# Optimization experiments

Hardware: AMD Instinct MI355X
Metric: run time of the kernel (lower is better)

Reference implementation:

```python
import jax, jax.numpy as jnp
import numpy as np

N = 50000      # nodes
E = 600000     # edges (avg degree 12)
D_IN = 16      # node_input_size
D = 128        # hidden_size
H = 4          # num_heads
DH = D // H
L = 4          # message_passing_num
D_FF = 512     # 4*hidden FFN expansion
D_OUT = 3      # output_size


def setup_inputs() -> dict:
    key = jax.random.key(0)
    ks = iter(jax.random.split(key, 32))
    def w(shape, fan_in):
        return jax.random.normal(next(ks), shape, jnp.float32) / np.float32(np.sqrt(fan_in))
    return {
        "features": jax.random.normal(next(ks), (N, D_IN), jnp.float32),
        "senders": jax.random.randint(next(ks), (E,), 0, N),
        "receivers": jax.random.randint(next(ks), (E,), 0, N),
        "enc_w1": w((D_IN, D), D_IN), "enc_b1": jnp.zeros((D,), jnp.float32),
        "enc_w2": w((D, D), D),       "enc_b2": jnp.zeros((D,), jnp.float32),
        "wq": w((L, D, D), D), "wk": w((L, D, D), D),
        "wv": w((L, D, D), D), "wo": w((L, D, D), D),
        "ln1_s": jnp.ones((L, D), jnp.float32), "ln1_b": jnp.zeros((L, D), jnp.float32),
        "ffn_w1": w((L, D, D_FF), D), "ffn_b1": jnp.zeros((L, D_FF), jnp.float32),
        "ffn_w2": w((L, D_FF, D), D_FF), "ffn_b2": jnp.zeros((L, D), jnp.float32),
        "ln2_s": jnp.ones((L, D), jnp.float32), "ln2_b": jnp.zeros((L, D), jnp.float32),
        "dec_w1": w((D, D_OUT), D), "dec_b1": jnp.zeros((D_OUT,), jnp.float32),
        "dec_w2": w((D_OUT, D_OUT), D_OUT), "dec_b2": jnp.zeros((D_OUT,), jnp.float32),
    }


def _ln(x, s, b):
    mu = x.mean(-1, keepdims=True)
    var = ((x - mu) ** 2).mean(-1, keepdims=True)
    return (x - mu) * jax.lax.rsqrt(var + 1e-5) * s + b


def _graph_mha(x, senders, receivers, wq, wk, wv, wo):
    # Adjacency-masked attention done sparsely over the edge list
    # (equivalent to softmax over the BCOO adjacency pattern).
    n = x.shape[0]
    q = (x @ wq).reshape(n, H, DH)
    k = (x @ wk).reshape(n, H, DH)
    v = (x @ wv).reshape(n, H, DH)
    scores = (q[receivers] * k[senders]).sum(-1) / np.float32(np.sqrt(DH))  # [E,H]
    m = jax.ops.segment_max(scores, receivers, num_segments=n)             # [N,H]
    m = jnp.where(jnp.isfinite(m), m, 0.0)
    a = jnp.exp(scores - m[receivers])                                      # [E,H]
    denom = jax.ops.segment_sum(a, receivers, num_segments=n)              # [N,H]
    msg = jax.ops.segment_sum(a[:, :, None] * v[senders], receivers, num_segments=n)  # [N,H,DH]
    out = (msg / (denom[:, :, None] + 1e-9)).reshape(n, D)
    return out @ wo


def reference(features, senders, receivers,
              enc_w1, enc_b1, enc_w2, enc_b2,
              wq, wk, wv, wo, ln1_s, ln1_b,
              ffn_w1, ffn_b1, ffn_w2, ffn_b2, ln2_s, ln2_b,
              dec_w1, dec_b1, dec_w2, dec_b2):
    # encode
    x = jnp.maximum(features @ enc_w1 + enc_b1, 0.0) @ enc_w2 + enc_b2     # [N,D]
    # process: L pre-LN sparse-attention transformer blocks
    for l in range(L):
        h = _ln(x, ln1_s[l], ln1_b[l])
        x = x + _graph_mha(h, senders, receivers, wq[l], wk[l], wv[l], wo[l])
        h = _ln(x, ln2_s[l], ln2_b[l])
        x = x + jnp.maximum(h @ ffn_w1[l] + ffn_b1[l], 0.0) @ ffn_w2[l] + ffn_b2[l]
    # decode
    return jnp.maximum(x @ dec_w1 + dec_b1, 0.0) @ dec_w2 + dec_b2         # [N,D_OUT]
```

## Files before the change

kernel.cpp:

```cpp
#include <hip/hip_runtime.h>
#include <hip/hip_bf16.h>
#include <math.h>

#define D     128
#define NHEAD 4
#define DH    32
#define DFF   512
#define DIN   16
#define MAXDEG 64
#define TN    16

typedef __attribute__((ext_vector_type(8))) short bf16x8;
typedef __attribute__((ext_vector_type(4))) float f32x4;
typedef __hip_bfloat16 bf16;

#define QSCALE_L2E 0.2550348838f


#define WAITV(N) asm volatile("s_waitcnt vmcnt(" #N ")" ::: "memory")
#define WAITLGKM asm volatile("s_waitcnt lgkmcnt(0)" ::: "memory")
#define FENCE()  asm volatile("" ::: "memory")
#define BAR() do { FENCE(); __builtin_amdgcn_s_barrier(); FENCE(); } while (0)

__device__ __forceinline__ void gll16(const bf16* g, bf16* l) {
    __builtin_amdgcn_global_load_lds((__attribute__((address_space(1))) void*)g,
                                     (__attribute__((address_space(3))) void*)l,
                                     16, 0, 0);
}

__device__ __forceinline__ ushort bfbits(float f) {
    __hip_bfloat16 b = __float2bfloat16(f);
    return *(ushort*)&b;
}

__global__ void k_fill(const int* __restrict__ recv, const int* __restrict__ senders,
                       int* __restrict__ deg, int* __restrict__ eid, int E) {
    int e = blockIdx.x * blockDim.x + threadIdx.x;
    if (e >= E) return;
    int r = recv[e];
    int pos = atomicAdd(&deg[r], 1);
    if (pos < MAXDEG) eid[r * MAXDEG + pos] = senders[e];
}

__global__ void k_wt(const float* __restrict__ wq, const float* __restrict__ wk,
                     const float* __restrict__ wv, const float* __restrict__ wo,
                     const float* __restrict__ w1, const float* __restrict__ w2,
                     const float* __restrict__ encw2,
                     bf16* __restrict__ wqkvT, bf16* __restrict__ woT,
                     bf16* __restrict__ w1T, bf16* __restrict__ w2T,
                     bf16* __restrict__ encw2T, int* __restrict__ deg,
                     int* __restrict__ eid, int N) {
    int r = blockIdx.y;
    if (r == 25) {
        int tot = N + N * MAXDEG;
        for (int i = blockIdx.x * blockDim.x + threadIdx.x; i < tot;
             i += 256 * 256) {
            if (i < N) deg[i] = 0;
            else eid[i - N] = 0;
        }
        return;
    }
    const float* src; bf16* dst; int K, Nout;
    if (r < 12) {
        int l = r / 3, sel = r % 3;
        src = (sel == 0 ? wq : sel == 1 ? wk : wv) + (size_t)l * D * D;
        dst = wqkvT + (size_t)l * 3 * D * D + (size_t)sel * D * D;
        K = D; Nout = D;
    } else if (r < 16) {
        int l = r - 12;
        src = wo + (size_t)l * D * D; dst = woT + (size_t)l * D * D; K = D; Nout = D;
    } else if (r < 20) {
        int l = r - 16;
        src = w1 + (size_t)l * D * DFF; dst = w1T + (size_t)l * D * DFF; K = D; Nout = DFF;
    } else if (r < 24) {
        int l = r - 20;
        src = w2 + (size_t)l * DFF * D; dst = w2T + (size_t)l * DFF * D; K = DFF; Nout = D;
    } else {
        src = encw2; dst = encw2T; K = D; Nout = D;
    }
    int total = K * Nout;
    int i = blockIdx.x * blockDim.x + threadIdx.x;
    if (i >= total) return;
    int k = i / Nout, j = i % Nout;
    dst[(size_t)j * K + k] = __float2bfloat16(src[i]);
}

__device__ __forceinline__ void load_afrag(const bf16* A, int arow, int quad,
                                           int N, bf16x8* afr) {
    const bf16* ab = A + (size_t)arow * D + quad * 8;
#pragma unroll
    for (int i = 0; i < 4; i++) {
        uint4 v = make_uint4(0u, 0u, 0u, 0u);
        if (arow < N) v = *(const uint4*)(ab + i * 32);
        afr[i] = *(bf16x8*)&v;
    }
}

__device__ __forceinline__ void stage_q(bf16* lb, const bf16* src, int rs,
                                        int wave, int lane) {
#pragma unroll
    for (int k = 0; k < 2; k++) {
        int gidx = (wave * 2 + k) * 64 + lane;
        int r = gidx >> 2, gL = gidx & 3;
        gll16(src + (size_t)r * rs + ((gL ^ ((r >> 1) & 3)) * 8),
              lb + (size_t)(wave * 2 + k) * 512);
    }
}

template<int OP>
__global__ __launch_bounds__(256) void k_gemm(
        const bf16* __restrict__ A, const bf16* __restrict__ Bt,
        const float* __restrict__ bias,
        const float* __restrict__ lns, const float* __restrict__ lnb,
        float* x, bf16* outB, int N) {
    __shared__ alignas(16) bf16 Wq4[4][32 * 128];
    int m0 = blockIdx.x * 64;
    int t = threadIdx.x;
    int wave = t >> 6, lane = t & 63;
    int quad = lane >> 4, l16 = lane & 15;
    int wm = wave * 16;
    int rowb = m0 + wm + quad * 4;

    float xv[8][4];
    if (OP == 2) {
#pragma unroll
        for (int j = 0; j < 8; j++)
#pragma unroll
            for (int r = 0; r < 4; r++) {
                int gr = rowb + r;
                xv[j][r] = (gr < N) ? x[(size_t)gr * D + j * 16 + l16] : 0.f;
            }
    }
    bf16x8 afr[4];
    load_afrag(A, m0 + wm + l16, quad, N, afr);
    FENCE();
#pragma unroll
    for (int p = 0; p < 4; p++) {
        stage_q(&Wq4[p][0], Bt + p * 32, 128, wave, lane);
        FENCE();
    }

    int wswz = (quad ^ ((l16 >> 1) & 3)) * 8;
    f32x4 acc[8];
#pragma unroll
    for (int j = 0; j < 8; j++) acc[j] = (f32x4){0.f, 0.f, 0.f, 0.f};
#pragma unroll
    for (int s = 0; s < 4; s++) {
        if (s == 0) { WAITV(6); } else if (s == 1) { WAITV(4); }
        else if (s == 2) { WAITV(2); } else { WAITV(0); }
        BAR();
        const bf16* Wb = &Wq4[s][0];
        __builtin_amdgcn_s_setprio(1);
#pragma unroll
        for (int j = 0; j < 8; j++) {
            const bf16* wp = Wb + (size_t)(j * 16 + l16) * 32 + wswz;
            acc[j] = __builtin_amdgcn_mfma_f32_16x16x32_bf16(
                afr[s], *(const bf16x8*)wp, acc[j], 0, 0, 0);
        }
        __builtin_amdgcn_s_setprio(0);
    }

    float bv[8];
    if (OP == 5) {
#pragma unroll
        for (int j = 0; j < 8; j++) bv[j] = bias[j * 16 + l16];
    }
#pragma unroll
    for (int j = 0; j < 8; j++) {
#pragma unroll
        for (int r = 0; r < 4; r++) {
            int gr = rowb + r;
            if (gr >= N) continue;
            float val = acc[j][r];
            if (OP == 5) val += bv[j];
            if (OP == 2) val += xv[j][r];
            acc[j][r] = val;
        }
    }
    float lsv[8], lbv[8];
#pragma unroll
    for (int j = 0; j < 8; j++) {
        lsv[j] = lns[j * 16 + l16];
        lbv[j] = lnb[j * 16 + l16];
    }
#pragma unroll
    for (int r = 0; r < 4; r++) {
        float s1 = 0.f, s2 = 0.f;
#pragma unroll
        for (int j = 0; j < 8; j++) {
            float v = acc[j][r];
            s1 += v; s2 += v * v;
        }
        s1 += __shfl_xor(s1, 1, 64);  s2 += __shfl_xor(s2, 1, 64);
        s1 += __shfl_xor(s1, 2, 64);  s2 += __shfl_xor(s2, 2, 64);
        s1 += __shfl_xor(s1, 4, 64);  s2 += __shfl_xor(s2, 4, 64);
        s1 += __shfl_xor(s1, 8, 64);  s2 += __shfl_xor(s2, 8, 64);
        float mu = s1 * (1.f / 128.f);
        float var = s2 * (1.f / 128.f) - mu * mu;
        float rinv = rsqrtf(fmaxf(var, 0.f) + 1e-5f);
        int gr = rowb + r;
        if (gr >= N) continue;
#pragma unroll
        for (int j = 0; j < 8; j++) {
            int col = j * 16 + l16;
            float v = acc[j][r];
            x[(size_t)gr * D + col] = v;
            outB[(size_t)gr * D + col] =
                __float2bfloat16((v - mu) * rinv * lsv[j] + lbv[j]);
        }
    }
}

__device__ __forceinline__ void stage_qkv_q(int ts, const bf16* wqkvT,
                                            bf16* Wb6, int wave, int lane) {
    int tsel = ts >> 2, p = ts & 3;
    size_t off = (tsel == 0) ? (size_t)D * D
               : (tsel == 1) ? (size_t)2 * D * D : 0;
    stage_q(Wb6 + (size_t)(ts % 6) * (32 * 128), wqkvT + off + p * 32, 128,
            wave, lane);
}

__global__ __launch_bounds__(256) void k_qkv(
        const bf16* __restrict__ hb, const bf16* __restrict__ wqkvT,
        bf16* __restrict__ qb, bf16* __restrict__ kvb, int N) {
    __shared__ alignas(16) bf16 Wb6[6][32 * 128];
    int m0 = blockIdx.x * 64;
    int t = threadIdx.x;
    int wave = t >> 6, lane = t & 63;
    int quad = lane >> 4, l16 = lane & 15;
    int wm = wave * 16;
    int rowb = m0 + wm + quad * 4;

    bf16x8 afr[4];
    load_afrag(hb, m0 + wm + l16, quad, N, afr);
    FENCE();
    stage_qkv_q(0, wqkvT, &Wb6[0][0], wave, lane); FENCE();
    stage_qkv_q(1, wqkvT, &Wb6[0][0], wave, lane); FENCE();
    stage_qkv_q(2, wqkvT, &Wb6[0][0], wave, lane); FENCE();
    stage_qkv_q(3, wqkvT, &Wb6[0][0], wave, lane); FENCE();

    int wswz = (quad ^ ((l16 >> 1) & 3)) * 8;
    f32x4 accK[8], accV[8], accQ[8];

#pragma unroll
    for (int s = 0; s < 12; s++) {
        if (s + 4 < 12) {
            stage_qkv_q(s + 4, wqkvT, &Wb6[0][0], wave, lane);
            FENCE();
        }
        if (s < 8)        { WAITV(8); }
        else if (s == 8)  { WAITV(6); }
        else if (s == 9)  { WAITV(4); }
        else if (s == 10) { WAITV(2); }
        else              { WAITV(0); }
        BAR();
        const bf16* Wb = &Wb6[0][0] + (size_t)(s % 6) * (32 * 128);
        int q = s & 3;
        __builtin_amdgcn_s_setprio(1);
#pragma unroll
        for (int j = 0; j < 8; j++) {
            const bf16* wp = Wb + (size_t)(j * 16 + l16) * 32 + wswz;
            if (s < 4) {
                if (q == 0) accK[j] = (f32x4){0.f, 0.f, 0.f, 0.f};
                accK[j] = __builtin_amdgcn_mfma_f32_16x16x32_bf16(
                    afr[q], *(const bf16x8*)wp, accK[j], 0, 0, 0);
            } else if (s < 8) {
                if (q == 0) accV[j] = (f32x4){0.f, 0.f, 0.f, 0.f};
                accV[j] = __builtin_amdgcn_mfma_f32_16x16x32_bf16(
                    afr[q], *(const bf16x8*)wp, accV[j], 0, 0, 0);
            } else {
                if (q == 0) accQ[j] = (f32x4){0.f, 0.f, 0.f, 0.f};
                accQ[j] = __builtin_amdgcn_mfma_f32_16x16x32_bf16(
                    afr[q], *(const bf16x8*)wp, accQ[j], 0, 0, 0);
            }
        }
        __builtin_amdgcn_s_setprio(0);
    }

#pragma unroll
    for (int j = 0; j < 8; j++) {
        int col = j * 16 + l16;
#pragma unroll
        for (int r = 0; r < 4; r++) {
            int gr = rowb + r;
            if (gr >= N) continue;
            uint kv = (uint)bfbits(accK[j][r]) | ((uint)bfbits(accV[j][r]) << 16);
            *(uint*)&kvb[((size_t)gr * D + col) * 2] = kv;
            qb[(size_t)gr * D + col] = __float2bfloat16(accQ[j][r] * QSCALE_L2E);
        }
    }
}

__device__ __forceinline__ void stage_ffn_q(int ts, const bf16* w1T,
                                            const bf16* w2T, bf16* Wb6,
                                            int wave, int lane) {
    int c = ts >> 3, p = ts & 7;
    const bf16* src; int rs;
    if (p < 4) { src = w1T + (size_t)(c * 128) * 128 + p * 32;       rs = 128; }
    else       { src = w2T + (size_t)(c * 128) + (p - 4) * 32;       rs = DFF; }
    stage_q(Wb6 + (size_t)(ts % 6) * (32 * 128), src, rs, wave, lane);
}

template<int MODE>
__global__ __launch_bounds__(256) void k_ffn(
        const bf16* __restrict__ hb, const bf16* __restrict__ w1T,
        const float* __restrict__ b1,
        const bf16* __restrict__ w2T, const float* __restrict__ b2,
        const float* __restrict__ lns, const float* __restrict__ lnb,
        const float* __restrict__ dw1, const float* __restrict__ db1,
        const float* __restrict__ dw2, const float* __restrict__ db2,
        float* x, bf16* outB, float* out, int N) {
    __shared__ alignas(16) bf16 Wb6[6][32 * 128];
    __shared__ alignas(16) bf16 Hsm[64 * 128];
    int m0 = blockIdx.x * 64;
    int t = threadIdx.x;
    int wave = t >> 6, lane = t & 63;
    int quad = lane >> 4, l16 = lane & 15;
    int wm = wave * 16;
    int rowb = m0 + wm + quad * 4;

    float b1pre[4][8];
#pragma unroll
    for (int c2 = 0; c2 < 4; c2++)
#pragma unroll
        for (int j = 0; j < 8; j++) b1pre[c2][j] = b1[c2 * 128 + j * 16 + l16];

    bf16x8 afr[4];
    load_afrag(hb, m0 + wm + l16, quad, N, afr);
    FENCE();
    stage_ffn_q(0, w1T, w2T, &Wb6[0][0], wave, lane); FENCE();
    stage_ffn_q(1, w1T, w2T, &Wb6[0][0], wave, lane); FENCE();
    stage_ffn_q(2, w1T, w2T, &Wb6[0][0], wave, lane); FENCE();
    stage_ffn_q(3, w1T, w2T, &Wb6[0][0], wave, lane); FENCE();

    f32x4 acc2[8], accP[8];
#pragma unroll
    for (int j = 0; j < 8; j++) acc2[j] = (f32x4){0.f, 0.f, 0.f, 0.f};
    float xv[8][4];

    int wswz = (quad ^ ((l16 >> 1) & 3)) * 8;

#pragma unroll
    for (int s = 0; s < 32; s++) {
        if (s + 4 < 32) {
            stage_ffn_q(s + 4, w1T, w2T, &Wb6[0][0], wave, lane);
            FENCE();
        }
        if (s < 28)       { WAITV(8); }
        else if (s == 28) { WAITV(6); }
        else if (s == 29) { WAITV(4); }
        else if (s == 30) { WAITV(2); }
        else              { WAITV(0); }
        BAR();
        if (s == 31) {
#pragma unroll
            for (int j = 0; j < 8; j++)
#pragma unroll
                for (int r = 0; r < 4; r++) {
                    int gr = min(rowb + r, N - 1);
                    xv[j][r] = x[(size_t)gr * D + j * 16 + l16];
                }
            FENCE();
        }
        const bf16* Wb = &Wb6[0][0] + (size_t)(s % 6) * (32 * 128);
        int c = s >> 3, p = s & 7;
        if (p < 4) {
            if (p == 0) {
#pragma unroll
                for (int j = 0; j < 8; j++) accP[j] = (f32x4){0.f, 0.f, 0.f, 0.f};
            }
            __builtin_amdgcn_s_setprio(1);
#pragma unroll
            for (int j = 0; j < 8; j++) {
                const bf16* wp = Wb + (size_t)(j * 16 + l16) * 32 + wswz;
                accP[j] = __builtin_amdgcn_mfma_f32_16x16x32_bf16(
                    afr[p], *(const bf16x8*)wp, accP[j], 0, 0, 0);
            }
            __builtin_amdgcn_s_setprio(0);
            if (p == 3) {
                int rw = wm + quad * 4;
#pragma unroll
                for (int j = 0; j < 8; j++) {
                    int gb = j * 2 + (l16 >> 3), ce = l16 & 7;
#pragma unroll
                    for (int r = 0; r < 4; r++) {
                        int row = rw + r;
                        Hsm[(size_t)row * 128 + (size_t)((gb ^ (row & 15)) * 8) + ce] =
                            __float2bfloat16(fmaxf(accP[j][r] + b1pre[c][j], 0.f));
                    }
                }
                WAITLGKM;
            }
        } else {
            int kq = p - 4;
            bf16x8 af2 = *(const bf16x8*)(Hsm + (size_t)(wm + l16) * 128
                              + (size_t)(((kq * 4 + quad) ^ l16) * 8));
            __builtin_amdgcn_s_setprio(1);
#pragma unroll
            for (int j = 0; j < 8; j++) {
                const bf16* wp = Wb + (size_t)(j * 16 + l16) * 32 + wswz;
                acc2[j] = __builtin_amdgcn_mfma_f32_16x16x32_bf16(
                    af2, *(const bf16x8*)wp, acc2[j], 0, 0, 0);
            }
            __builtin_amdgcn_s_setprio(0);
        }
    }
    WAITV(0);
    FENCE();

    float bv[8];
#pragma unroll
    for (int j = 0; j < 8; j++) bv[j] = b2[j * 16 + l16];
#pragma unroll
    for (int j = 0; j < 8; j++) {
#pragma unroll
        for (int r = 0; r < 4; r++) {
            int gr = rowb + r;
            if (gr >= N) continue;
            acc2[j][r] += bv[j] + xv[j][r];
        }
    }
    if (MODE == 1) {
        float dw[8][3];
#pragma unroll
        for (int j = 0; j < 8; j++) {
            int col = j * 16 + l16;
#pragma unroll
            for (int cc3 = 0; cc3 < 3; cc3++) dw[j][cc3] = dw1[col * 3 + cc3];
        }
#pragma unroll
        for (int r = 0; r < 4; r++) {
            float s0 = 0.f, s1 = 0.f, s2 = 0.f;
#pragma unroll
            for (int j = 0; j < 8; j++) {
                float v = acc2[j][r];
                s0 += v * dw[j][0]; s1 += v * dw[j][1]; s2 += v * dw[j][2];
            }
            s0 += __shfl_xor(s0, 1, 64); s1 += __shfl_xor(s1, 1, 64); s2 += __shfl_xor(s2, 1, 64);
            s0 += __shfl_xor(s0, 2, 64); s1 += __shfl_xor(s1, 2, 64); s2 += __shfl_xor(s2, 2, 64);
            s0 += __shfl_xor(s0, 4, 64); s1 += __shfl_xor(s1, 4, 64); s2 += __shfl_xor(s2, 4, 64);
            s0 += __shfl_xor(s0, 8, 64); s1 += __shfl_xor(s1, 8, 64); s2 += __shfl_xor(s2, 8, 64);
            int gr = rowb + r;
            if (l16 == 0 && gr < N) {
                float t0 = fmaxf(s0 + db1[0], 0.f);
                float t1 = fmaxf(s1 + db1[1], 0.f);
                float t2 = fmaxf(s2 + db1[2], 0.f);
#pragma unroll
                for (int o = 0; o < 3; o++)
                    out[(size_t)gr * 3 + o] =
                        t0 * dw2[0 * 3 + o] + t1 * dw2[1 * 3 + o] + t2 * dw2[2 * 3 + o] + db2[o];
            }
        }
        return;
    }
    float lsv[8], lbv[8];
#pragma unroll
    for (int j = 0; j < 8; j++) {
        lsv[j] = lns[j * 16 + l16];
        lbv[j] = lnb[j * 16 + l16];
    }
#pragma unroll
    for (int r = 0; r < 4; r++) {
        float s1 = 0.f, s2 = 0.f;
#pragma unroll
        for (int j = 0; j < 8; j++) {
            float v = acc2[j][r];
            s1 += v; s2 += v * v;
        }
        s1 += __shfl_xor(s1, 1, 64);  s2 += __shfl_xor(s2, 1, 64);
        s1 += __shfl_xor(s1, 2, 64);  s2 += __shfl_xor(s2, 2, 64);
        s1 += __shfl_xor(s1, 4, 64);  s2 += __shfl_xor(s2, 4, 64);
        s1 += __shfl_xor(s1, 8, 64);  s2 += __shfl_xor(s2, 8, 64);
        float mu = s1 * (1.f / 128.f);
        float var = s2 * (1.f / 128.f) - mu * mu;
        float rinv = rsqrtf(fmaxf(var, 0.f) + 1e-5f);
        int gr = rowb + r;
        if (gr >= N) continue;
#pragma unroll
        for (int j = 0; j < 8; j++) {
            int col = j * 16 + l16;
            float v = acc2[j][r];
            x[(size_t)gr * D + col] = v;
            outB[(size_t)gr * D + col] = __float2bfloat16((v - mu) * rinv * lsv[j] + lbv[j]);
        }
    }
}

__global__ void k_enc1(const float* __restrict__ feat,
                       const float* __restrict__ w1, const float* __restrict__ b1,
                       bf16* __restrict__ hb, int N) {
    __shared__ float fsh[TN][DIN];
    int n0 = blockIdx.x * TN;
    int j = threadIdx.x;
    int nvalid = min(TN, N - n0);
    for (int idx = j; idx < TN * DIN; idx += 128) {
        int n = idx / DIN, i = idx % DIN;
        fsh[n][i] = (n < nvalid) ? feat[(n0 + n) * DIN + i] : 0.f;
    }
    __syncthreads();
    float bb = b1[j];
#pragma unroll
    for (int n = 0; n < TN; n++) {
        float a = bb;
#pragma unroll
        for (int i = 0; i < DIN; i++) a += fsh[n][i] * w1[i * D + j];
        if (n < nvalid) hb[(size_t)(n0 + n) * D + j] = __float2bfloat16(fmaxf(a, 0.f));
    }
}

__device__ __forceinline__ void attn_edge(uint4 w, bool v, float4 qv,
                                          float& l, float& a0, float& a1,
                                          float& a2, float& a3) {
    float k0 = __uint_as_float(w.x << 16), v0 = __uint_as_float(w.x & 0xFFFF0000u);
    float k1 = __uint_as_float(w.y << 16), v1 = __uint_as_float(w.y & 0xFFFF0000u);
    float k2 = __uint_as_float(w.z << 16), v2 = __uint_as_float(w.z & 0xFFFF0000u);
    float k3 = __uint_as_float(w.w << 16), v3 = __uint_as_float(w.w & 0xFFFF0000u);
    float p = qv.x * k0 + qv.y * k1 + qv.z * k2 + qv.w * k3;
    p += __shfl_xor(p, 1, 64);
    p += __shfl_xor(p, 2, 64);
    p += __shfl_xor(p, 4, 64);
    float e = v ? exp2f(p) : 0.f;
    l += e;
    a0 += e * v0; a1 += e * v1; a2 += e * v2; a3 += e * v3;
}

__device__ __forceinline__ float4 unpackq(uint2 qw) {
    float4 qv;
    qv.x = __uint_as_float(qw.x << 16);
    qv.y = __uint_as_float(qw.x & 0xFFFF0000u);
    qv.z = __uint_as_float(qw.y << 16);
    qv.w = __uint_as_float(qw.y & 0xFFFF0000u);
    return qv;
}

__global__ __launch_bounds__(256) void k_attn(
        const bf16* __restrict__ qb, const uint* __restrict__ kvb,
        const int* __restrict__ deg, const int* __restrict__ eid,
        bf16* __restrict__ out, int N) {
    int wave = threadIdx.x >> 6, lane = threadIdx.x & 63;
    int g = lane & 7, h = (lane >> 3) & 3, slot = lane >> 5;
    int d0 = h * 32 + g * 4;
    int rbase = blockIdx.x * 16 + wave * 4;
    if (rbase >= N) return;
    const uint* kvbase = kvb + d0;

    int ssN[8];
    {
        const int* row = eid + (size_t)rbase * MAXDEG;
#pragma unroll
        for (int u = 0; u < 8; u++) ssN[u] = row[u * 2 + slot];
    }
    int cntN = min(deg[rbase], MAXDEG);
    float4 qvN = unpackq(*(const uint2*)(qb + (size_t)rbase * D + d0));

#pragma unroll
    for (int i = 0; i < 4; i++) {
        int r = rbase + i;
        if (r >= N) return;
        int cnt = cntN; float4 qv = qvN;
        uint4 w[8];
#pragma unroll
        for (int u = 0; u < 8; u++)
            w[u] = *(const uint4*)(kvbase + (size_t)ssN[u] * D);
        int rn = r + 1;
        if (i < 3 && rn < N) {
            const int* rowN = eid + (size_t)rn * MAXDEG;
#pragma unroll
            for (int u = 0; u < 8; u++) ssN[u] = rowN[u * 2 + slot];
            cntN = min(deg[rn], MAXDEG);
            qvN = unpackq(*(const uint2*)(qb + (size_t)rn * D + d0));
        }
        float l = 0.f, a0 = 0.f, a1 = 0.f, a2 = 0.f, a3 = 0.f;
#pragma unroll
        for (int u = 0; u < 8; u++)
            attn_edge(w[u], (u * 2 + slot) < cnt, qv, l, a0, a1, a2, a3);
        for (int base = 16; base < cnt; base += 16) {
            const int* row = eid + (size_t)r * MAXDEG;
            int ss[8]; bool vv[8];
#pragma unroll
            for (int u = 0; u < 8; u++) {
                int e = base + u * 2 + slot;
                vv[u] = e < cnt;
                ss[u] = row[e];
            }
            uint4 w2_[8];
#pragma unroll
            for (int u = 0; u < 8; u++)
                w2_[u] = *(const uint4*)(kvbase + (size_t)ss[u] * D);
#pragma unroll
            for (int u = 0; u < 8; u++)
                attn_edge(w2_[u], vv[u], qv, l, a0, a1, a2, a3);
        }
        l  += __shfl_xor(l, 32, 64);
        a0 += __shfl_xor(a0, 32, 64);
        a1 += __shfl_xor(a1, 32, 64);
        a2 += __shfl_xor(a2, 32, 64);
        a3 += __shfl_xor(a3, 32, 64);
        if (lane < 32) {
            float inv = 1.f / (l + 1e-9f);
            bf16 o[4];
            o[0] = __float2bfloat16(a0 * inv);
            o[1] = __float2bfloat16(a1 * inv);
            o[2] = __float2bfloat16(a2 * inv);
            o[3] = __float2bfloat16(a3 * inv);
            *(uint2*)(out + (size_t)r * D + d0) = *(uint2*)o;
        }
    }
}

extern "C" void kernel_launch(void* const* d_in, const int* in_sizes, int n_in,
                              void* d_out, int out_size, void* d_ws, size_t ws_size,
                              hipStream_t stream) {
    const float* feat    = (const float*)d_in[0];
    const int*   senders = (const int*)d_in[1];
    const int*   recv    = (const int*)d_in[2];
    const float* enc_w1  = (const float*)d_in[3];
    const float* enc_b1  = (const float*)d_in[4];
    const float* enc_w2  = (const float*)d_in[5];
    const float* enc_b2  = (const float*)d_in[6];
    const float* wq      = (const float*)d_in[7];
    const float* wk      = (const float*)d_in[8];
    const float* wv      = (const float*)d_in[9];
    const float* wo      = (const float*)d_in[10];
    const float* ln1_s   = (const float*)d_in[11];
    const float* ln1_b   = (const float*)d_in[12];
    const float* ffn_w1  = (const float*)d_in[13];
    const float* ffn_b1  = (const float*)d_in[14];
    const float* ffn_w2  = (const float*)d_in[15];
    const float* ffn_b2  = (const float*)d_in[16];
    const float* ln2_s   = (const float*)d_in[17];
    const float* ln2_b   = (const float*)d_in[18];
    const float* dec_w1  = (const float*)d_in[19];
    const float* dec_b1  = (const float*)d_in[20];
    const float* dec_w2  = (const float*)d_in[21];
    const float* dec_b2  = (const float*)d_in[22];

    int N = in_sizes[0] / DIN;
    int E = in_sizes[1];

    char* p = (char*)d_ws;
    float* x   = (float*)p;  p += (size_t)N * D * 4;
    bf16*  qb  = (bf16*)p;   p += (size_t)N * D * 2;
    bf16*  kvb = (bf16*)p;   p += (size_t)N * D * 2 * 2;
    bf16*  hb  = (bf16*)p;   p += (size_t)N * D * 2;
    int* deg   = (int*)p;    p += (size_t)N * 4;
    int* eid   = (int*)p;    p += (size_t)N * MAXDEG * 4;
    bf16* wqkvT  = (bf16*)p; p += (size_t)4 * 3 * D * D * 2;
    bf16* woT    = (bf16*)p; p += (size_t)4 * D * D * 2;
    bf16* w1T    = (bf16*)p; p += (size_t)4 * D * DFF * 2;
    bf16* w2T    = (bf16*)p; p += (size_t)4 * DFF * D * 2;
    bf16* encw2T = (bf16*)p; p += (size_t)D * D * 2;

    int gm64 = (N + 63) / 64;

    k_wt<<<dim3(256, 26), 256, 0, stream>>>(wq, wk, wv, wo, ffn_w1, ffn_w2, enc_w2,
                                            wqkvT, woT, w1T, w2T, encw2T, deg, eid, N);
    k_fill<<<(E + 255) / 256, 256, 0, stream>>>(recv, senders, deg, eid, E);
    k_enc1<<<(N + TN - 1) / TN, 128, 0, stream>>>(feat, enc_w1, enc_b1, hb, N);
    k_gemm<5><<<gm64, 256, 0, stream>>>(hb, encw2T, enc_b2, ln1_s, ln1_b, x, hb, N);

    for (int l = 0; l < 4; l++) {
        k_qkv<<<gm64, 256, 0, stream>>>(hb, wqkvT + (size_t)l * 3 * D * D, qb, kvb, N);
        k_attn<<<(N + 15) / 16, 256, 0, stream>>>(qb, (const uint*)kvb, deg, eid, hb, N);
        k_gemm<2><<<gm64, 256, 0, stream>>>(hb, woT + (size_t)l * D * D,
                                            nullptr, ln2_s + l * D, ln2_b + l * D,
                                            x, hb, N);
        if (l < 3)
            k_ffn<0><<<gm64, 256, 0, stream>>>(hb, w1T + (size_t)l * D * DFF,
                                               ffn_b1 + l * DFF,
                                               w2T + (size_t)l * DFF * D, ffn_b2 + l * D,
                                               ln1_s + (l + 1) * D, ln1_b + (l + 1) * D,
                                               nullptr, nullptr, nullptr, nullptr,
                                               x, hb, nullptr, N);
        else
            k_ffn<1><<<gm64, 256, 0, stream>>>(hb, w1T + (size_t)l * D * DFF,
                                               ffn_b1 + l * DFF,
                                               w2T + (size_t)l * DFF * D, ffn_b2 + l * D,
                                               nullptr, nullptr,
                                               dec_w1, dec_b1, dec_w2, dec_b2,
                                               x, nullptr, (float*)d_out, N);
    }
}
```

Before: 636.3 us.

## Fuse output projection and LN2 into the FFN kernel

Folds the attention output projection (wo GEMM), residual add and second LayerNorm into the FFN kernel. The normalized activations stay in shared memory instead of making a round trip through global memory, and one launch per layer goes away. The weight pipeline is extended from 32 to 36 stages, and the kernel gains a second 16KB shared buffer, which may lower occupancy. The residual x row is now read once at the start and held in registers, so register pressure rises.

```diff
diff --git a/kernel.cpp b/kernel.cpp
--- a/kernel.cpp
+++ b/kernel.cpp
@@ -291,27 +291,32 @@
     }
 }
 
-__device__ __forceinline__ void stage_ffn_q(int ts, const bf16* w1T,
-                                            const bf16* w2T, bf16* Wb6,
-                                            int wave, int lane) {
-    int c = ts >> 3, p = ts & 7;
+__device__ __forceinline__ void stage_wff_q(int ts, const bf16* woT,
+                                            const bf16* w1T, const bf16* w2T,
+                                            bf16* Wb6, int wave, int lane) {
     const bf16* src; int rs;
-    if (p < 4) { src = w1T + (size_t)(c * 128) * 128 + p * 32;       rs = 128; }
-    else       { src = w2T + (size_t)(c * 128) + (p - 4) * 32;       rs = DFF; }
+    if (ts < 4) { src = woT + ts * 32; rs = 128; }
+    else {
+        int q = ts - 4, c = q >> 3, p = q & 7;
+        if (p < 4) { src = w1T + (size_t)(c * 128) * 128 + p * 32; rs = 128; }
+        else       { src = w2T + (size_t)(c * 128) + (p - 4) * 32; rs = DFF; }
+    }
     stage_q(Wb6 + (size_t)(ts % 6) * (32 * 128), src, rs, wave, lane);
 }
 
 template<int MODE>
-__global__ __launch_bounds__(256) void k_ffn(
-        const bf16* __restrict__ hb, const bf16* __restrict__ w1T,
-        const float* __restrict__ b1,
+__global__ __launch_bounds__(256) void k_wff(
+        const bf16* __restrict__ hb, const bf16* __restrict__ woT,
+        const float* __restrict__ ln2s, const float* __restrict__ ln2b,
+        const bf16* __restrict__ w1T, const float* __restrict__ b1,
         const bf16* __restrict__ w2T, const float* __restrict__ b2,
         const float* __restrict__ lns, const float* __restrict__ lnb,
         const float* __restrict__ dw1, const float* __restrict__ db1,
         const float* __restrict__ dw2, const float* __restrict__ db2,
         float* x, bf16* outB, float* out, int N) {
     __shared__ alignas(16) bf16 Wb6[6][32 * 128];
-    __shared__ alignas(16) bf16 Hsm[64 * 128];
+    __shared__ alignas(16) bf16 HsmA[64 * 128];
+    __shared__ alignas(16) bf16 HsmH[64 * 128];
     int m0 = blockIdx.x * 64;
     int t = threadIdx.x;
     int wave = t >> 6, lane = t & 63;
@@ -319,107 +324,150 @@
     int wm = wave * 16;
     int rowb = m0 + wm + quad * 4;
 
-    float b1pre[4][8];
+    float l2s[8], l2b[8], b1pre[4][8];
+#pragma unroll
+    for (int j = 0; j < 8; j++) {
+        l2s[j] = ln2s[j * 16 + l16];
+        l2b[j] = ln2b[j * 16 + l16];
+    }
 #pragma unroll
     for (int c2 = 0; c2 < 4; c2++)
 #pragma unroll
         for (int j = 0; j < 8; j++) b1pre[c2][j] = b1[c2 * 128 + j * 16 + l16];
-
+    float xv[8][4];
+#pragma unroll
+    for (int j = 0; j < 8; j++)
+#pragma unroll
+        for (int r = 0; r < 4; r++) {
+            int gr = min(rowb + r, N - 1);
+            xv[j][r] = x[(size_t)gr * D + j * 16 + l16];
+        }
     bf16x8 afr[4];
     load_afrag(hb, m0 + wm + l16, quad, N, afr);
     FENCE();
-    stage_ffn_q(0, w1T, w2T, &Wb6[0][0], wave, lane); FENCE();
-    stage_ffn_q(1, w1T, w2T, &Wb6[0][0], wave, lane); FENCE();
-    stage_ffn_q(2, w1T, w2T, &Wb6[0][0], wave, lane); FENCE();
-    stage_ffn_q(3, w1T, w2T, &Wb6[0][0], wave, lane); FENCE();
-
-    f32x4 acc2[8], accP[8];
-#pragma unroll
-    for (int j = 0; j < 8; j++) acc2[j] = (f32x4){0.f, 0.f, 0.f, 0.f};
-    float xv[8][4];
+    stage_wff_q(0, woT, w1T, w2T, &Wb6[0][0], wave, lane); FENCE();
+    stage_wff_q(1, woT, w1T, w2T, &Wb6[0][0], wave, lane); FENCE();
+    stage_wff_q(2, woT, w1T, w2T, &Wb6[0][0], wave, lane); FENCE();
+    stage_wff_q(3, woT, w1T, w2T, &Wb6[0][0], wave, lane); FENCE();
 
     int wswz = (quad ^ ((l16 >> 1) & 3)) * 8;
-
-#pragma unroll
-    for (int s = 0; s < 32; s++) {
-        if (s + 4 < 32) {
-            stage_ffn_q(s + 4, w1T, w2T, &Wb6[0][0], wave, lane);
+    f32x4 accP[8], acc2[8];
+    float val[8][4];
+#pragma unroll
+    for (int j = 0; j < 8; j++) accP[j] = (f32x4){0.f, 0.f, 0.f, 0.f};
+
+#pragma unroll
+    for (int s = 0; s < 36; s++) {
+        if (s + 4 < 36) {
+            stage_wff_q(s + 4, woT, w1T, w2T, &Wb6[0][0], wave, lane);
             FENCE();
         }
-        if (s < 28)       { WAITV(8); }
-        else if (s == 28) { WAITV(6); }
-        else if (s == 29) { WAITV(4); }
-        else if (s == 30) { WAITV(2); }
+        if (s < 32)       { WAITV(8); }
+        else if (s == 32) { WAITV(6); }
+        else if (s == 33) { WAITV(4); }
+        else if (s == 34) { WAITV(2); }
         else              { WAITV(0); }
         BAR();
-        if (s == 31) {
-#pragma unroll
-            for (int j = 0; j < 8; j++)
-#pragma unroll
-                for (int r = 0; r < 4; r++) {
-                    int gr = min(rowb + r, N - 1);
-                    xv[j][r] = x[(size_t)gr * D + j * 16 + l16];
-                }
-            FENCE();
-        }
         const bf16* Wb = &Wb6[0][0] + (size_t)(s % 6) * (32 * 128);
-        int c = s >> 3, p = s & 7;
-        if (p < 4) {
-            if (p == 0) {
-#pragma unroll
-                for (int j = 0; j < 8; j++) accP[j] = (f32x4){0.f, 0.f, 0.f, 0.f};
-            }
+        if (s < 4) {
             __builtin_amdgcn_s_setprio(1);
 #pragma unroll
             for (int j = 0; j < 8; j++) {
                 const bf16* wp = Wb + (size_t)(j * 16 + l16) * 32 + wswz;
                 accP[j] = __builtin_amdgcn_mfma_f32_16x16x32_bf16(
-                    afr[p], *(const bf16x8*)wp, accP[j], 0, 0, 0);
+                    afr[s], *(const bf16x8*)wp, accP[j], 0, 0, 0);
             }
             __builtin_amdgcn_s_setprio(0);
-            if (p == 3) {
+            if (s == 3) {
+#pragma unroll
+                for (int j = 0; j < 8; j++)
+#pragma unroll
+                    for (int r = 0; r < 4; r++)
+                        val[j][r] = accP[j][r] + xv[j][r];
                 int rw = wm + quad * 4;
 #pragma unroll
-                for (int j = 0; j < 8; j++) {
-                    int gb = j * 2 + (l16 >> 3), ce = l16 & 7;
-#pragma unroll
-                    for (int r = 0; r < 4; r++) {
-                        int row = rw + r;
-                        Hsm[(size_t)row * 128 + (size_t)((gb ^ (row & 15)) * 8) + ce] =
-                            __float2bfloat16(fmaxf(accP[j][r] + b1pre[c][j], 0.f));
+                for (int r = 0; r < 4; r++) {
+                    float s1 = 0.f, s2 = 0.f;
+#pragma unroll
+                    for (int j = 0; j < 8; j++) {
+                        float v = val[j][r];
+                        s1 += v; s2 += v * v;
+                    }
+                    s1 += __shfl_xor(s1, 1, 64);  s2 += __shfl_xor(s2, 1, 64);
+                    s1 += __shfl_xor(s1, 2, 64);  s2 += __shfl_xor(s2, 2, 64);
+                    s1 += __shfl_xor(s1, 4, 64);  s2 += __shfl_xor(s2, 4, 64);
+                    s1 += __shfl_xor(s1, 8, 64);  s2 += __shfl_xor(s2, 8, 64);
+                    float mu = s1 * (1.f / 128.f);
+                    float var = s2 * (1.f / 128.f) - mu * mu;
+                    float rinv = rsqrtf(fmaxf(var, 0.f) + 1e-5f);
+                    int row = rw + r;
+#pragma unroll
+                    for (int j = 0; j < 8; j++) {
+                        int gb = j * 2 + (l16 >> 3), ce = l16 & 7;
+                        HsmA[(size_t)row * 128 + (size_t)((gb ^ (row & 15)) * 8) + ce] =
+                            __float2bfloat16((val[j][r] - mu) * rinv * l2s[j] + l2b[j]);
                     }
                 }
                 WAITLGKM;
+#pragma unroll
+                for (int j = 0; j < 8; j++) acc2[j] = (f32x4){0.f, 0.f, 0.f, 0.f};
             }
         } else {
-            int kq = p - 4;
-            bf16x8 af2 = *(const bf16x8*)(Hsm + (size_t)(wm + l16) * 128
-                              + (size_t)(((kq * 4 + quad) ^ l16) * 8));
-            __builtin_amdgcn_s_setprio(1);
-#pragma unroll
-            for (int j = 0; j < 8; j++) {
-                const bf16* wp = Wb + (size_t)(j * 16 + l16) * 32 + wswz;
-                acc2[j] = __builtin_amdgcn_mfma_f32_16x16x32_bf16(
-                    af2, *(const bf16x8*)wp, acc2[j], 0, 0, 0);
+            int q = s - 4, c = q >> 3, p = q & 7;
+            if (p < 4) {
+                if (p == 0) {
+#pragma unroll
+                    for (int j = 0; j < 8; j++) accP[j] = (f32x4){0.f, 0.f, 0.f, 0.f};
+                }
+                bf16x8 afA = *(const bf16x8*)(HsmA + (size_t)(wm + l16) * 128
+                                  + (size_t)(((p * 4 + quad) ^ l16) * 8));
+                __builtin_amdgcn_s_setprio(1);
+#pragma unroll
+                for (int j = 0; j < 8; j++) {
+                    const bf16* wp = Wb + (size_t)(j * 16 + l16) * 32 + wswz;
+                    accP[j] = __builtin_amdgcn_mfma_f32_16x16x32_bf16(
+                        afA, *(const bf16x8*)wp, accP[j], 0, 0, 0);
+                }
+                __builtin_amdgcn_s_setprio(0);
+                if (p == 3) {
+                    int rw = wm + quad * 4;
+#pragma unroll
+                    for (int j = 0; j < 8; j++) {
+                        int gb = j * 2 + (l16 >> 3), ce = l16 & 7;
+#pragma unroll
+                        for (int r = 0; r < 4; r++) {
+                            int row = rw + r;
+                            HsmH[(size_t)row * 128 + (size_t)((gb ^ (row & 15)) * 8) + ce] =
+                                __float2bfloat16(fmaxf(accP[j][r] + b1pre[c][j], 0.f));
+                        }
+                    }
+                    WAITLGKM;
+                }
+            } else {
+                int kq = p - 4;
+                bf16x8 afH = *(const bf16x8*)(HsmH + (size_t)(wm + l16) * 128
+                                  + (size_t)(((kq * 4 + quad) ^ l16) * 8));
+                __builtin_amdgcn_s_setprio(1);
+#pragma unroll
+                for (int j = 0; j < 8; j++) {
+                    const bf16* wp = Wb + (size_t)(j * 16 + l16) * 32 + wswz;
+                    acc2[j] = __builtin_amdgcn_mfma_f32_16x16x32_bf16(
+                        afH, *(const bf16x8*)wp, acc2[j], 0, 0, 0);
+                }
+                __builtin_amdgcn_s_setprio(0);
             }
-            __builtin_amdgcn_s_setprio(0);
-        }
-    }
-    WAITV(0);
-    FENCE();
+        }
+    }
 
     float bv[8];
 #pragma unroll
     for (int j = 0; j < 8; j++) bv[j] = b2[j * 16 + l16];
 #pragma unroll
-    for (int j = 0; j < 8; j++) {
-#pragma unroll
-        for (int r = 0; r < 4; r++) {
-            int gr = rowb + r;
-            if (gr >= N) continue;
-            acc2[j][r] += bv[j] + xv[j][r];
-        }
-    }
+    for (int j = 0; j < 8; j++)
+#pragma unroll
+        for (int r = 0; r < 4; r++)
+            acc2[j][r] += bv[j] + val[j][r];
+
     if (MODE == 1) {
         float dw[8][3];
 #pragma unroll
@@ -662,18 +710,19 @@
     for (int l = 0; l < 4; l++) {
         k_qkv<<<gm64, 256, 0, stream>>>(hb, wqkvT + (size_t)l * 3 * D * D, qb, kvb, N);
         k_attn<<<(N + 15) / 16, 256, 0, stream>>>(qb, (const uint*)kvb, deg, eid, hb, N);
-        k_gemm<2><<<gm64, 256, 0, stream>>>(hb, woT + (size_t)l * D * D,
-                                            nullptr, ln2_s + l * D, ln2_b + l * D,
-                                            x, hb, N);
         if (l < 3)
-            k_ffn<0><<<gm64, 256, 0, stream>>>(hb, w1T + (size_t)l * D * DFF,
+            k_wff<0><<<gm64, 256, 0, stream>>>(hb, woT + (size_t)l * D * D,
+                                               ln2_s + l * D, ln2_b + l * D,
+                                               w1T + (size_t)l * D * DFF,
                                                ffn_b1 + l * DFF,
                                                w2T + (size_t)l * DFF * D, ffn_b2 + l * D,
                                                ln1_s + (l + 1) * D, ln1_b + (l + 1) * D,
                                                nullptr, nullptr, nullptr, nullptr,
                                                x, hb, nullptr, N);
         else
-            k_ffn<1><<<gm64, 256, 0, stream>>>(hb, w1T + (size_t)l * D * DFF,
+            k_wff<1><<<gm64, 256, 0, stream>>>(hb, woT + (size_t)l * D * D,
+                                               ln2_s + l * D, ln2_b + l * D,
+                                               w1T + (size_t)l * D * DFF,
                                                ffn_b1 + l * DFF,
                                                w2T + (size_t)l * DFF * D, ffn_b2 + l * D,
                                                nullptr, nullptr,
```

New measurement: 634.8 us. About the same (-0.2%).
